# Kernel tuning notes

Hardware: AMD Instinct MI355X
Metric: run time of the kernel (lower is better)

The kernel has to match this reference:

```python
import jax, jax.numpy as jnp
import numpy as np

D_EMBED = 1024
D_HEAD = 128


def setup_inputs() -> dict:
    key = jax.random.key(0)
    kx, kq, kk, kv = jax.random.split(key, 4)
    x = jax.random.normal(kx, (4, 4096, D_EMBED), dtype=jnp.float32)
    # nn.Linear(d_embed, d_head, bias=False) weights, stored [out, in] like torch
    s = 1.0 / np.sqrt(D_EMBED)
    Wq = jax.random.uniform(kq, (D_HEAD, D_EMBED), jnp.float32, -s, s)
    Wk = jax.random.uniform(kk, (D_HEAD, D_EMBED), jnp.float32, -s, s)
    Wv = jax.random.uniform(kv, (D_HEAD, D_EMBED), jnp.float32, -s, s)
    return {"x": x, "Wq": Wq, "Wk": Wk, "Wv": Wv}


def reference(x, Wq, Wk, Wv):
    # q,k,v: [b, s, d_head]
    q = jnp.einsum("bse,he->bsh", x, Wq)
    k = jnp.einsum("bse,he->bsh", x, Wk)
    v = jnp.einsum("bse,he->bsh", x, Wv)
    # original: (q @ k^T) * d_head**-0.5, then divided by sqrt(d_embed)
    scale = 1.0 / (np.sqrt(D_HEAD) * np.sqrt(D_EMBED))
    scores = jnp.einsum("bqh,bkh->bqk", q, k) * jnp.float32(scale)  # [b, s, s]
    attn = jax.nn.softmax(scores, axis=-1)
    return jnp.einsum("bqk,bkh->bqh", attn, v)
```

## Files before the change

kernel.cpp:

```cpp
#include <hip/hip_runtime.h>
#include <stdint.h>

typedef __bf16 bf16x8 __attribute__((ext_vector_type(8)));
typedef float  f32x4  __attribute__((ext_vector_type(4)));

#define ATTN_SCALE 2.7621359e-3f

__device__ __forceinline__ unsigned short f2bf(float f) {
  union { float f; uint32_t u; } v; v.f = f;
  uint32_t u = v.u;
  uint32_t r = (u + 0x7FFFu + ((u >> 16) & 1u)) >> 16;
  return (unsigned short)r;
}

__device__ __forceinline__ void load_lds16(const unsigned short* g, unsigned short* l) {
  __builtin_amdgcn_global_load_lds(
      (const __attribute__((address_space(1))) void*)g,
      (__attribute__((address_space(3))) void*)l, 16, 0, 0);
}

__device__ __forceinline__ f32x4 mfma16(bf16x8 a, bf16x8 b, f32x4 c) {
  return __builtin_amdgcn_mfma_f32_16x16x32_bf16(a, b, c, 0, 0, 0);
}

__device__ __forceinline__ bf16x8 ones_bf16() {
  union { unsigned short u[8]; bf16x8 v; } c;
#pragma unroll
  for (int j = 0; j < 8; ++j) c.u[j] = 0x3F80;
  return c.v;
}

__global__ __launch_bounds__(256, 3) void k_proj(
    const float* __restrict__ X,
    const float* __restrict__ Wq,
    const float* __restrict__ Wk,
    const float* __restrict__ Wv,
    unsigned short* __restrict__ Qb,
    unsigned short* __restrict__ Kb,
    unsigned short* __restrict__ Vt)
{
  __shared__ __align__(16) unsigned short sm[2048 + 4096];
  unsigned short* As = sm;
  unsigned short* Bs = sm + 2048;
  const int t = threadIdx.x;
  const int mtile = blockIdx.x;
  const int nt = blockIdx.y;
  const int w = t >> 6, lane = t & 63, quad = lane >> 4, l15 = lane & 15;
  const int wm = w & 1, wn = w >> 1;

  const float* Wsel = (nt == 0) ? Wq : (nt == 1) ? Wk : Wv;

  const float* ag0 = X + (size_t)(mtile * 64 + (t >> 2)) * 1024 + (t & 3) * 8;
  const float* bg0 = Wsel + (size_t)(t >> 2) * 1024 + (t & 3) * 8;
  unsigned short* aw = &As[t * 8];
  unsigned short* bw = &Bs[t * 8];

  f32x4 acc[2][4] = {};

  float4 a0 = *(const float4*)(ag0);
  float4 a1 = *(const float4*)(ag0 + 4);
  float4 b0 = *(const float4*)(bg0);
  float4 b1 = *(const float4*)(bg0 + 4);
  float4 b2 = *(const float4*)(bg0 + 65536);
  float4 b3 = *(const float4*)(bg0 + 65536 + 4);

  for (int kt = 0; kt < 32; ++kt) {
    asm volatile("s_waitcnt lgkmcnt(0)" ::: "memory");
    asm volatile("s_barrier" ::: "memory");

    float4 na0 = a0, na1 = a1, nb0 = b0, nb1 = b1, nb2 = b2, nb3 = b3;
    if (kt < 31) {
      na0 = *(const float4*)(ag0 + (kt + 1) * 32);
      na1 = *(const float4*)(ag0 + (kt + 1) * 32 + 4);
      nb0 = *(const float4*)(bg0 + (kt + 1) * 32);
      nb1 = *(const float4*)(bg0 + (kt + 1) * 32 + 4);
      nb2 = *(const float4*)(bg0 + (kt + 1) * 32 + 65536);
      nb3 = *(const float4*)(bg0 + (kt + 1) * 32 + 65536 + 4);
    }

    {
      union { unsigned short u[8]; uint4 v; } pa;
      pa.u[0] = f2bf(a0.x); pa.u[1] = f2bf(a0.y);
      pa.u[2] = f2bf(a0.z); pa.u[3] = f2bf(a0.w);
      pa.u[4] = f2bf(a1.x); pa.u[5] = f2bf(a1.y);
      pa.u[6] = f2bf(a1.z); pa.u[7] = f2bf(a1.w);
      *(uint4*)aw = pa.v;
      union { unsigned short u[8]; uint4 v; } pb;
      pb.u[0] = f2bf(b0.x); pb.u[1] = f2bf(b0.y);
      pb.u[2] = f2bf(b0.z); pb.u[3] = f2bf(b0.w);
      pb.u[4] = f2bf(b1.x); pb.u[5] = f2bf(b1.y);
      pb.u[6] = f2bf(b1.z); pb.u[7] = f2bf(b1.w);
      *(uint4*)bw = pb.v;
      pb.u[0] = f2bf(b2.x); pb.u[1] = f2bf(b2.y);
      pb.u[2] = f2bf(b2.z); pb.u[3] = f2bf(b2.w);
      pb.u[4] = f2bf(b3.x); pb.u[5] = f2bf(b3.y);
      pb.u[6] = f2bf(b3.z); pb.u[7] = f2bf(b3.w);
      *(uint4*)(bw + 2048) = pb.v;
    }

    asm volatile("s_waitcnt lgkmcnt(0)" ::: "memory");
    asm volatile("s_barrier" ::: "memory");

    bf16x8 af[2], bfr[4];
#pragma unroll
    for (int i = 0; i < 2; ++i)
      af[i] = *(const bf16x8*)&As[(wm * 32 + i * 16 + l15) * 32 + quad * 8];
#pragma unroll
    for (int j = 0; j < 4; ++j)
      bfr[j] = *(const bf16x8*)&Bs[(wn * 64 + j * 16 + l15) * 32 + quad * 8];
#pragma unroll
    for (int i = 0; i < 2; ++i)
#pragma unroll
      for (int j = 0; j < 4; ++j)
        acc[i][j] = mfma16(af[i], bfr[j], acc[i][j]);

    a0 = na0; a1 = na1; b0 = nb0; b1 = nb1; b2 = nb2; b3 = nb3;
  }

  if (nt != 2) {
    const int m0 = mtile * 64 + wm * 32;
#pragma unroll
    for (int i = 0; i < 2; ++i)
#pragma unroll
      for (int j = 0; j < 4; ++j)
#pragma unroll
        for (int r = 0; r < 4; ++r) {
          int m = m0 + i * 16 + quad * 4 + r;
          int n = wn * 64 + j * 16 + l15;
          float v = acc[i][j][r];
          if (nt == 0) Qb[(size_t)m * 128 + n] = f2bf(v * ATTN_SCALE);
          else         Kb[(size_t)m * 128 + n] = f2bf(v);
        }
  } else {
    float* Ts = (float*)sm;
    const int bb = mtile >> 6;
    const int s0 = (mtile & 63) * 64;
#pragma unroll
    for (int jj = 0; jj < 8; ++jj) {
      __syncthreads();
      if (wn == (jj >> 2)) {
        const int j = jj & 3;
#pragma unroll
        for (int i = 0; i < 2; ++i)
#pragma unroll
          for (int r = 0; r < 4; ++r)
            Ts[(wm * 32 + i * 16 + quad * 4 + r) * 17 + l15] = acc[i][j][r];
      }
      __syncthreads();
      int n2 = jj * 16 + (t >> 4);
      int m2 = (t & 15) * 4;
      union { unsigned short u[4]; uint2 v; } pk;
#pragma unroll
      for (int e = 0; e < 4; ++e) pk.u[e] = f2bf(Ts[(m2 + e) * 17 + (t >> 4)]);
      *(uint2*)&Vt[((size_t)(bb * 128 + n2)) * 4096 + s0 + m2] = pk.v;
    }
  }
}

__global__ __launch_bounds__(256, 3) void k_flash(
    const unsigned short* __restrict__ Qb,
    const unsigned short* __restrict__ Kb,
    const unsigned short* __restrict__ Vt,
    float* __restrict__ Om,
    float* __restrict__ lp)
{
  __shared__ __align__(16) unsigned short smem[21504];
  unsigned short* Psh = smem + 16384;
  float* Ob  = (float*)smem;
  float* lsh = (float*)(smem + 16384);

  const int t = threadIdx.x;
  const int w = t >> 6, lane = t & 63, quad = lane >> 4, l15 = lane & 15;
  const int h = w & 1, p = w >> 1;
  const int bid = blockIdx.x;
  const int b   = (bid & 7) >> 1;
  const int sp  = bid & 1;
  const int qt  = bid >> 3;

  const unsigned short* Qg = Qb + (size_t)(b * 4096 + qt * 64 + h * 32) * 128;
  const unsigned short* Kg = Kb + (size_t)b * 4096 * 128;
  const unsigned short* Vg = Vt + (size_t)b * 128 * 4096;

  bf16x8 qf[2][4];
#pragma unroll
  for (int mt = 0; mt < 2; ++mt)
#pragma unroll
    for (int kk = 0; kk < 4; ++kk)
      qf[mt][kk] = *(const bf16x8*)&Qg[(size_t)(mt * 16 + l15) * 128 + kk * 32 + quad * 8];

  f32x4 O[2][8] = {};
  f32x4 Ol[2] = {};

  const unsigned short* kg0 = Kg + (size_t)(t >> 4) * 128 + (((t & 15) ^ ((t >> 5) & 7)) * 8);
  const unsigned short* vg0 = Vg + (size_t)(t >> 3) * 4096 + (((t & 7) ^ ((t >> 3) & 7)) * 8);
  unsigned short* kw = &smem[w * 512];
  unsigned short* vw = &smem[8192 + w * 512];

  const int kt0 = sp * 32;

  {
    const unsigned short* kg = kg0 + (size_t)kt0 * 8192;
#pragma unroll
    for (int it = 0; it < 4; ++it)
      load_lds16(kg + it * 2048, kw + it * 2048);
  }

  for (int i = 0; i < 32; ++i) {
    const int kt = kt0 + i;
    const int ktn = (i < 31) ? (kt + 1) : kt0;

    asm volatile("s_waitcnt vmcnt(0)" ::: "memory");
    asm volatile("s_barrier" ::: "memory");

    {
      const unsigned short* vg = vg0 + (size_t)kt * 64;
#pragma unroll
      for (int it = 0; it < 4; ++it)
        load_lds16(vg + (size_t)it * 131072, vw + it * 2048);
    }

    f32x4 sc[2][2] = {};
#pragma unroll
    for (int ntk = 0; ntk < 2; ++ntk) {
      const int row = p * 32 + 2 * l15 + ntk;
#pragma unroll
      for (int kk = 0; kk < 4; ++kk) {
        bf16x8 kf = *(const bf16x8*)&smem[row * 128 + (((kk * 4 + quad) ^ (l15 & 7)) * 8)];
        sc[0][ntk] = mfma16(qf[0][kk], kf, sc[0][ntk]);
        sc[1][ntk] = mfma16(qf[1][kk], kf, sc[1][ntk]);
      }
    }

#pragma unroll
    for (int mt = 0; mt < 2; ++mt)
#pragma unroll
      for (int r = 0; r < 4; ++r) {
        float e0 = __expf(sc[mt][0][r]);
        float e1 = __expf(sc[mt][1][r]);
        int row = mt * 16 + quad * 4 + r;
        uint32_t pk = (uint32_t)f2bf(e0) | ((uint32_t)f2bf(e1) << 16);
        *(uint32_t*)&Psh[w * 1280 + row * 40 + 2 * l15] = pk;
      }

    asm volatile("s_waitcnt vmcnt(0) lgkmcnt(0)" ::: "memory");
    asm volatile("s_barrier" ::: "memory");

    {
      const unsigned short* kg = kg0 + (size_t)ktn * 8192;
#pragma unroll
      for (int it = 0; it < 4; ++it)
        load_lds16(kg + it * 2048, kw + it * 2048);
    }

    bf16x8 pf0 = *(const bf16x8*)&Psh[w * 1280 + l15 * 40 + quad * 8];
    bf16x8 pf1 = *(const bf16x8*)&Psh[w * 1280 + (16 + l15) * 40 + quad * 8];
    const bf16x8 one = ones_bf16();
    Ol[0] = mfma16(pf0, one, Ol[0]);
    Ol[1] = mfma16(pf1, one, Ol[1]);
    const unsigned short* Vshc = &smem[8192];
#pragma unroll
    for (int dt = 0; dt < 8; ++dt) {
      bf16x8 vf = *(const bf16x8*)&Vshc[(dt * 16 + l15) * 64 + (((p * 4 + quad) ^ (l15 & 7)) * 8)];
      O[0][dt] = mfma16(pf0, vf, O[0][dt]);
      O[1][dt] = mfma16(pf1, vf, O[1][dt]);
    }
  }

  __syncthreads();
  if (p == 1) {
#pragma unroll
    for (int mt = 0; mt < 2; ++mt)
#pragma unroll
      for (int r = 0; r < 4; ++r) {
        int row = h * 32 + mt * 16 + quad * 4 + r;
        if (l15 == 0) lsh[row] = Ol[mt][r];
#pragma unroll
        for (int dt = 0; dt < 8; ++dt)
          Ob[row * 128 + dt * 16 + l15] = O[mt][dt][r];
      }
  }
  __syncthreads();
  if (p == 0) {
    const size_t rowbase = (size_t)b * 4096 + qt * 64;
    float* Omp = Om + (size_t)sp * 2097152;
#pragma unroll
    for (int mt = 0; mt < 2; ++mt)
#pragma unroll
      for (int r = 0; r < 4; ++r) {
        int row = h * 32 + mt * 16 + quad * 4 + r;
#pragma unroll
        for (int dt = 0; dt < 8; ++dt)
          Omp[(rowbase + row) * 128 + dt * 16 + l15] =
              O[mt][dt][r] + Ob[row * 128 + dt * 16 + l15];
        if (l15 == 0)
          lp[(size_t)sp * 16384 + rowbase + row] = Ol[mt][r] + lsh[row];
      }
  }
}

__global__ __launch_bounds__(256) void k_merge(const float* __restrict__ Om,
                                               const float* __restrict__ lp,
                                               float* __restrict__ out) {
  int i = blockIdx.x * 256 + threadIdx.x;
  int row = i >> 5;
  float inv = 1.0f / (lp[row] + lp[16384 + row]);
  float4 a = ((const float4*)Om)[i];
  float4 c = ((const float4*)Om)[524288 + i];
  float4 o;
  o.x = (a.x + c.x) * inv;
  o.y = (a.y + c.y) * inv;
  o.z = (a.z + c.z) * inv;
  o.w = (a.w + c.w) * inv;
  ((float4*)out)[i] = o;
}

extern "C" void kernel_launch(void* const* d_in, const int* in_sizes, int n_in,
                              void* d_out, int out_size, void* d_ws, size_t ws_size,
                              hipStream_t stream) {
  const float* x  = (const float*)d_in[0];
  const float* Wq = (const float*)d_in[1];
  const float* Wk = (const float*)d_in[2];
  const float* Wv = (const float*)d_in[3];
  float* out = (float*)d_out;

  unsigned short* ws  = (unsigned short*)d_ws;
  unsigned short* Qb  = ws;
  unsigned short* Kb  = Qb + 2097152;
  unsigned short* Vt  = Kb + 2097152;
  float* Om = (float*)(Vt + 2097152);
  float* lp = Om + 4194304;

  k_proj<<<dim3(256, 3), 256, 0, stream>>>(x, Wq, Wk, Wv, Qb, Kb, Vt);
  k_flash<<<512, 256, 0, stream>>>(Qb, Kb, Vt, Om, lp);
  k_merge<<<2048, 256, 0, stream>>>(Om, lp, out);
}
```

Measured before the change: 175.6 us.

## Keep P in registers by computing transposed scores with permuted K layout

Computes S^T = K·Q^T with K rows loaded into LDS in a permuted order, so each lane's MFMA accumulator outputs already form the bf16x8 A-operand fragment for the P·V MFMA. This removes the P round trip through shared memory (write, then read back) and shrinks the LDS allocation, which could raise occupancy. K LDS reads also become contiguous per lane instead of XOR-swizzled. The risk is bank conflicts from the new K read and write pattern, and correctness depends on the row permutation matching the accumulator layout.

```diff
diff --git a/kernel.cpp b/kernel.cpp
--- a/kernel.cpp
+++ b/kernel.cpp
@@ -164,8 +164,7 @@
     float* __restrict__ Om,
     float* __restrict__ lp)
 {
-  __shared__ __align__(16) unsigned short smem[21504];
-  unsigned short* Psh = smem + 16384;
+  __shared__ __align__(16) unsigned short smem[16512];
   float* Ob  = (float*)smem;
   float* lsh = (float*)(smem + 16384);
 
@@ -191,19 +190,25 @@
   f32x4 O[2][8] = {};
   f32x4 Ol[2] = {};
 
-  const unsigned short* kg0 = Kg + (size_t)(t >> 4) * 128 + (((t & 15) ^ ((t >> 5) & 7)) * 8);
+  const unsigned short* ks[4];
+#pragma unroll
+  for (int it = 0; it < 4; ++it) {
+    const int r   = it * 4 + w;
+    const int row = (r >> 3) * 32 + (l15 >> 2) * 8 + (l15 & 3) + ((r >> 2) & 1) * 4;
+    const int col = ((r & 3) * 4 + quad) * 8;
+    ks[it] = Kg + (size_t)row * 128 + col;
+  }
+  unsigned short* kw = &smem[w * 512];
+  const unsigned short* kread = &smem[p * 4096 + lane * 8];
+
   const unsigned short* vg0 = Vg + (size_t)(t >> 3) * 4096 + (((t & 7) ^ ((t >> 3) & 7)) * 8);
-  unsigned short* kw = &smem[w * 512];
   unsigned short* vw = &smem[8192 + w * 512];
 
   const int kt0 = sp * 32;
 
-  {
-    const unsigned short* kg = kg0 + (size_t)kt0 * 8192;
-#pragma unroll
-    for (int it = 0; it < 4; ++it)
-      load_lds16(kg + it * 2048, kw + it * 2048);
-  }
+#pragma unroll
+  for (int it = 0; it < 4; ++it)
+    load_lds16(ks[it] + (size_t)kt0 * 8192, kw + it * 2048);
 
   for (int i = 0; i < 32; ++i) {
     const int kt = kt0 + i;
@@ -219,50 +224,44 @@
         load_lds16(vg + (size_t)it * 131072, vw + it * 2048);
     }
 
-    f32x4 sc[2][2] = {};
-#pragma unroll
-    for (int ntk = 0; ntk < 2; ++ntk) {
-      const int row = p * 32 + 2 * l15 + ntk;
+    f32x4 sc2[2][2] = {};
+#pragma unroll
+    for (int s = 0; s < 2; ++s)
 #pragma unroll
       for (int kk = 0; kk < 4; ++kk) {
-        bf16x8 kf = *(const bf16x8*)&smem[row * 128 + (((kk * 4 + quad) ^ (l15 & 7)) * 8)];
-        sc[0][ntk] = mfma16(qf[0][kk], kf, sc[0][ntk]);
-        sc[1][ntk] = mfma16(qf[1][kk], kf, sc[1][ntk]);
+        bf16x8 kf = *(const bf16x8*)&kread[(s * 4 + kk) * 512];
+        sc2[s][0] = mfma16(kf, qf[0][kk], sc2[s][0]);
+        sc2[s][1] = mfma16(kf, qf[1][kk], sc2[s][1]);
       }
-    }
-
-#pragma unroll
-    for (int mt = 0; mt < 2; ++mt)
-#pragma unroll
-      for (int r = 0; r < 4; ++r) {
-        float e0 = __expf(sc[mt][0][r]);
-        float e1 = __expf(sc[mt][1][r]);
-        int row = mt * 16 + quad * 4 + r;
-        uint32_t pk = (uint32_t)f2bf(e0) | ((uint32_t)f2bf(e1) << 16);
-        *(uint32_t*)&Psh[w * 1280 + row * 40 + 2 * l15] = pk;
-      }
+
+    bf16x8 pf[2];
+#pragma unroll
+    for (int mt = 0; mt < 2; ++mt) {
+      union { unsigned short u[8]; bf16x8 v; } pk;
+#pragma unroll
+      for (int s = 0; s < 2; ++s)
+#pragma unroll
+        for (int r = 0; r < 4; ++r)
+          pk.u[s * 4 + r] = f2bf(__expf(sc2[s][mt][r]));
+      pf[mt] = pk.v;
+    }
 
     asm volatile("s_waitcnt vmcnt(0) lgkmcnt(0)" ::: "memory");
     asm volatile("s_barrier" ::: "memory");
 
-    {
-      const unsigned short* kg = kg0 + (size_t)ktn * 8192;
-#pragma unroll
-      for (int it = 0; it < 4; ++it)
-        load_lds16(kg + it * 2048, kw + it * 2048);
-    }
-
-    bf16x8 pf0 = *(const bf16x8*)&Psh[w * 1280 + l15 * 40 + quad * 8];
-    bf16x8 pf1 = *(const bf16x8*)&Psh[w * 1280 + (16 + l15) * 40 + quad * 8];
+#pragma unroll
+    for (int it = 0; it < 4; ++it)
+      load_lds16(ks[it] + (size_t)ktn * 8192, kw + it * 2048);
+
     const bf16x8 one = ones_bf16();
-    Ol[0] = mfma16(pf0, one, Ol[0]);
-    Ol[1] = mfma16(pf1, one, Ol[1]);
+    Ol[0] = mfma16(pf[0], one, Ol[0]);
+    Ol[1] = mfma16(pf[1], one, Ol[1]);
     const unsigned short* Vshc = &smem[8192];
 #pragma unroll
     for (int dt = 0; dt < 8; ++dt) {
       bf16x8 vf = *(const bf16x8*)&Vshc[(dt * 16 + l15) * 64 + (((p * 4 + quad) ^ (l15 & 7)) * 8)];
-      O[0][dt] = mfma16(pf0, vf, O[0][dt]);
-      O[1][dt] = mfma16(pf1, vf, O[1][dt]);
+      O[0][dt] = mfma16(pf[0], vf, O[0][dt]);
+      O[1][dt] = mfma16(pf[1], vf, O[1][dt]);
     }
   }
 
```

Measured after the change: 181.3 us. 1.03x slower.
